# Kernel optimization log

Hardware: AMD Instinct MI355X
Metric: run time of the kernel (lower is better)

Reference implementation:

```python
import jax, jax.numpy as jnp
import numpy as np

N_NODES = 100000
N_FEATS = 256
OUT_DIM = 64
NNZ_X = 1280000
N_EDGES = 1600000
KEEP_PROB = 0.9  # 1 - dropout_rate (dropout_rate = 0.1)


def setup_inputs() -> dict:
    key = jax.random.key(0)
    ks = jax.random.split(key, 7)
    feat_values = jax.random.normal(ks[0], (NNZ_X,), dtype=jnp.float32)
    feat_rows = jax.random.randint(ks[1], (NNZ_X,), 0, N_NODES, dtype=jnp.int32)
    feat_cols = jax.random.randint(ks[2], (NNZ_X,), 0, N_FEATS, dtype=jnp.int32)
    # GlorotNormal kernel: std = sqrt(2 / (fan_in + fan_out))
    glorot_std = float(np.sqrt(2.0 / (N_FEATS + OUT_DIM)))
    kernel = jax.random.normal(ks[3], (N_FEATS, OUT_DIM), dtype=jnp.float32) * glorot_std
    adj_values = jax.random.uniform(ks[4], (N_EDGES,), dtype=jnp.float32)
    adj_rows = jax.random.randint(ks[5], (N_EDGES,), 0, N_NODES, dtype=jnp.int32)
    adj_cols = jax.random.randint(ks[6], (N_EDGES,), 0, N_NODES, dtype=jnp.int32)
    return {
        "feat_values": feat_values,
        "kernel": kernel,
        "adj_values": adj_values,
        "feat_rows": feat_rows,
        "feat_cols": feat_cols,
        "adj_rows": adj_rows,
        "adj_cols": adj_cols,
    }


def reference(feat_values, kernel, adj_values, feat_rows, feat_cols, adj_rows, adj_cols):
    # sparse dropout on feature values (training=True path), deterministic key.
    # tf: keep = floor(keep_prob + U[0,1)) cast to bool; retain then scale 1/keep_prob
    u = jax.random.uniform(jax.random.key(42), feat_values.shape, dtype=feat_values.dtype)
    keep = jnp.floor(KEEP_PROB + u).astype(bool)
    v = jnp.where(keep, feat_values, jnp.zeros_like(feat_values)) * (1.0 / KEEP_PROB)

    # SpMM 1: XW[n, o] = sum_{(n,f) in X} v * kernel[f, o]
    xw = jax.ops.segment_sum(v[:, None] * kernel[feat_cols], feat_rows,
                             num_segments=N_NODES)  # [N, OUT]

    # SpMM 2: out[i, o] = sum_{(i,j) in A} a_ij * xw[j, o]
    agg = jax.ops.segment_sum(adj_values[:, None] * xw[adj_cols], adj_rows,
                              num_segments=N_NODES)  # [N, OUT]

    return jax.nn.relu(agg)
```

## Files before the change

### kernel.cpp

```cpp
#include <hip/hip_runtime.h>

#define N_NODES 100000
#define N_FEATS 256
#define OUT_DIM 64
#define NNZ_X   1280000
#define N_EDGES 1600000
#define NB      391
#define CHUNK   4096
#define KPT     8
#define CAPX    4352
#define CAPA    5120

__device__ __forceinline__ unsigned rotl32(unsigned x, unsigned d) {
    return (x << d) | (x >> (32u - d));
}

__device__ __forceinline__ float jax_uniform_42(unsigned e) {
    unsigned x0 = 0u, x1 = e;
    const unsigned ks0 = 0u, ks1 = 42u, ks2 = 0u ^ 42u ^ 0x1BD11BDAu;
    x0 += ks0; x1 += ks1;
#define TF_R(r) { x0 += x1; x1 = rotl32(x1, r); x1 ^= x0; }
    TF_R(13) TF_R(15) TF_R(26) TF_R(6)
    x0 += ks1; x1 += ks2 + 1u;
    TF_R(17) TF_R(29) TF_R(16) TF_R(24)
    x0 += ks2; x1 += ks0 + 2u;
    TF_R(13) TF_R(15) TF_R(26) TF_R(6)
    x0 += ks0; x1 += ks1 + 3u;
    TF_R(17) TF_R(29) TF_R(16) TF_R(24)
    x0 += ks1; x1 += ks2 + 4u;
    TF_R(13) TF_R(15) TF_R(26) TF_R(6)
    x0 += ks2; x1 += ks0 + 5u;
#undef TF_R
    unsigned bits = x0 ^ x1;
    return __uint_as_float((bits >> 9) | 0x3f800000u) - 1.0f;
}

__device__ __forceinline__ bool keep_42(unsigned e) {
    float u = jax_uniform_42(e);
    return floorf(0.9f + u) != 0.0f;
}

__device__ __forceinline__ unsigned short f32_bf16(float f) {
    unsigned bits = __float_as_uint(f);
    return (unsigned short)((bits + 0x7fffu + ((bits >> 16) & 1u)) >> 16);
}

__device__ __forceinline__ float bf16_f32(unsigned short u) {
    return __uint_as_float((unsigned)u << 16);
}

__device__ __forceinline__ float bflo(unsigned u) { return __uint_as_float(u << 16); }
__device__ __forceinline__ float bfhi(unsigned u) { return __uint_as_float(u & 0xffff0000u); }

__global__ __launch_bounds__(512) void phase1(
        const float* __restrict__ fvals, const int* __restrict__ frows,
        const int* __restrict__ fcols,
        const float* __restrict__ avals, const int* __restrict__ arows,
        const int* __restrict__ acols,
        int* __restrict__ bcur_x, int* __restrict__ bcur_a,
        float2* __restrict__ gx, float2* __restrict__ ga) {
    const int isA = blockIdx.y;
    const float* vals = isA ? avals : fvals;
    const int* rows   = isA ? arows : frows;
    const int* cols   = isA ? acols : fcols;
    int* bcur         = isA ? bcur_a : bcur_x;
    float2* dst       = isA ? ga : gx;
    const unsigned cap = isA ? CAPA : CAPX;
    const unsigned n  = isA ? N_EDGES : NNZ_X;

    unsigned t = threadIdx.x;
    unsigned base = blockIdx.x * CHUNK;
    if (base >= n) return;

    __shared__ int cnt[512];
    __shared__ int start[512];
    __shared__ int cur[512];
    __shared__ int gbase[NB];
    __shared__ int wtot[8];
    __shared__ int s_nvalid;
    __shared__ unsigned long long payload[CHUNK];
    __shared__ unsigned short bkt[CHUNK];

    int   rcache[KPT];
    float vcache[KPT];
    int   ccache[KPT];

    cnt[t] = 0;
    __syncthreads();
    #pragma unroll
    for (int k = 0; k < KPT; k++) {
        unsigned i = base + k * 512u + t;
        int r = -1;
        if (i < n) {
            int rr = rows[i];
            float v = vals[i];
            int   c = cols[i];
            if (isA || keep_42(i)) {
                r = rr;
                vcache[k] = isA ? v : v * (float)(1.0 / 0.9);
                ccache[k] = c;
            }
        }
        rcache[k] = r;
        if (r >= 0) atomicAdd(&cnt[(unsigned)r >> 8], 1);
    }
    __syncthreads();
    unsigned lane = t & 63u, wid = t >> 6;
    int binv = cnt[t];
    int inc = binv;
    #pragma unroll
    for (int d = 1; d < 64; d <<= 1) {
        int v = __shfl_up(inc, d, 64);
        if (lane >= (unsigned)d) inc += v;
    }
    if (lane == 63u) wtot[wid] = inc;
    __syncthreads();
    int offw = 0;
    #pragma unroll
    for (int w = 0; w < 8; w++) if ((unsigned)w < wid) offw += wtot[w];
    int excl = offw + inc - binv;
    start[t] = excl;
    cur[t]   = excl;
    if (t == 511u) s_nvalid = excl + binv;
    if (t < NB) {
        int cb = cnt[t];
        if (cb > 0) gbase[t] = atomicAdd(&bcur[t], cb);
    }
    __syncthreads();
    int n_valid = s_nvalid;
    #pragma unroll
    for (int k = 0; k < KPT; k++) {
        int r = rcache[k];
        if (r >= 0) {
            unsigned b = (unsigned)r >> 8;
            int p = atomicAdd(&cur[b], 1);
            unsigned packed = ((unsigned)ccache[k] << 8) | ((unsigned)r & 255u);
            payload[p] = ((unsigned long long)__float_as_uint(vcache[k]) << 32) | packed;
            bkt[p] = (unsigned short)b;
        }
    }
    __syncthreads();
    #pragma unroll
    for (int k = 0; k < KPT; k++) {
        int sidx = k * 512 + (int)t;
        if (sidx < n_valid) {
            unsigned b = bkt[sidx];
            unsigned long long m = payload[sidx];
            float2 e;
            e.x = __uint_as_float((unsigned)(m >> 32));
            e.y = __int_as_float((int)(unsigned)m);
            dst[(size_t)b * cap + gbase[b] + (sidx - start[b])] = e;
        }
    }
}

__global__ __launch_bounds__(512) void sort_stage(
        const int* __restrict__ bcur_x, const float2* __restrict__ gx,
        const float* __restrict__ W, unsigned short* __restrict__ xw,
        const int* __restrict__ bcur_a, float2* __restrict__ ga,
        unsigned short* __restrict__ rs) {
    __shared__ float2 ent[CAPX];
    __shared__ int hist[256];
    __shared__ int starts[256];
    __shared__ int cursor[256];
    __shared__ int wtot[4];
    unsigned t = threadIdx.x;
    unsigned wid = t >> 6, lane = t & 63u;
    const int isA = (blockIdx.x >= NB);
    unsigned b = isA ? (blockIdx.x - NB) : blockIdx.x;

    if (!isA) {
        int cnt = bcur_x[b];
        const float2* src = gx + (size_t)b * CAPX;
        if (t < 256) hist[t] = 0;
        __syncthreads();
        for (int i = (int)t; i < cnt; i += 512)
            atomicAdd(&hist[((unsigned)__float_as_int(src[i].y)) & 255u], 1);
        __syncthreads();
        int inc = 0, binv = 0;
        if (wid < 4u) {
            unsigned bin = wid * 64u + lane;
            binv = hist[bin];
            inc = binv;
            #pragma unroll
            for (int d = 1; d < 64; d <<= 1) {
                int v = __shfl_up(inc, d, 64);
                if (lane >= (unsigned)d) inc += v;
            }
            if (lane == 63u) wtot[wid] = inc;
        }
        __syncthreads();
        if (wid < 4u) {
            int offw = 0;
            #pragma unroll
            for (int w = 0; w < 4; w++) if ((unsigned)w < wid) offw += wtot[w];
            unsigned bin = wid * 64u + lane;
            int excl = inc - binv + offw;
            starts[bin] = excl;
            cursor[bin] = excl;
        }
        __syncthreads();
        for (int i = (int)t; i < cnt; i += 512) {
            float2 e = src[i];
            int pos = atomicAdd(&cursor[((unsigned)__float_as_int(e.y)) & 255u], 1);
            ent[pos] = e;
        }
        __syncthreads();
        unsigned quarter = lane >> 4, sub = lane & 15u;
        const float4* W4 = (const float4*)W;
        ushort4* xw4 = (ushort4*)xw;
        for (unsigned r = wid; r < 256u; r += 8u) {
            int s0 = starts[r];
            int s1 = (r == 255u) ? cnt : starts[r + 1];
            float4 acc[4];
            #pragma unroll
            for (int j = 0; j < 4; j++) { acc[j].x = acc[j].y = acc[j].z = acc[j].w = 0.0f; }
            int p = s0;
            for (; p + 16 <= s1; p += 16) {
                float2 e[4];
                #pragma unroll
                for (int j = 0; j < 4; j++) e[j] = ent[p + 4 * quarter + j];
                float4 w[4];
                #pragma unroll
                for (int j = 0; j < 4; j++)
                    w[j] = W4[(((unsigned)__float_as_int(e[j].y)) >> 8) * 16u + sub];
                #pragma unroll
                for (int j = 0; j < 4; j++) {
                    acc[j].x = fmaf(e[j].x, w[j].x, acc[j].x);
                    acc[j].y = fmaf(e[j].x, w[j].y, acc[j].y);
                    acc[j].z = fmaf(e[j].x, w[j].z, acc[j].z);
                    acc[j].w = fmaf(e[j].x, w[j].w, acc[j].w);
                }
            }
            for (int q = p + (int)quarter; q < s1; q += 4) {
                float2 e = ent[q];
                float4 w = W4[(((unsigned)__float_as_int(e.y)) >> 8) * 16u + sub];
                acc[0].x = fmaf(e.x, w.x, acc[0].x);
                acc[0].y = fmaf(e.x, w.y, acc[0].y);
                acc[0].z = fmaf(e.x, w.z, acc[0].z);
                acc[0].w = fmaf(e.x, w.w, acc[0].w);
            }
            float ax = (acc[0].x + acc[1].x) + (acc[2].x + acc[3].x);
            float ay = (acc[0].y + acc[1].y) + (acc[2].y + acc[3].y);
            float az = (acc[0].z + acc[1].z) + (acc[2].z + acc[3].z);
            float aw = (acc[0].w + acc[1].w) + (acc[2].w + acc[3].w);
            ax += __shfl(ax, (int)(lane ^ 16u), 64);
            ay += __shfl(ay, (int)(lane ^ 16u), 64);
            az += __shfl(az, (int)(lane ^ 16u), 64);
            aw += __shfl(aw, (int)(lane ^ 16u), 64);
            ax += __shfl(ax, (int)(lane ^ 32u), 64);
            ay += __shfl(ay, (int)(lane ^ 32u), 64);
            az += __shfl(az, (int)(lane ^ 32u), 64);
            aw += __shfl(aw, (int)(lane ^ 32u), 64);
            unsigned grow = (b << 8) + r;
            if (quarter == 0 && grow < N_NODES) {
                ushort4 o;
                o.x = f32_bf16(ax); o.y = f32_bf16(ay);
                o.z = f32_bf16(az); o.w = f32_bf16(aw);
                xw4[(size_t)grow * 16u + sub] = o;
            }
        }
    } else {
        int cnt = bcur_a[b];
        float2* g = ga + (size_t)b * CAPA;
        if (t < 256) hist[t] = 0;
        __syncthreads();
        float2 ec[10];
        #pragma unroll
        for (int k = 0; k < 10; k++) {
            int i = k * 512 + (int)t;
            if (i < cnt) {
                float2 e = g[i];
                ec[k] = e;
                atomicAdd(&hist[((unsigned)__float_as_int(e.y)) & 255u], 1);
            }
        }
        __syncthreads();
        int inc = 0, binv = 0;
        if (wid < 4u) {
            unsigned bin = wid * 64u + lane;
            binv = hist[bin];
            inc = binv;
            #pragma unroll
            for (int d = 1; d < 64; d <<= 1) {
                int v = __shfl_up(inc, d, 64);
                if (lane >= (unsigned)d) inc += v;
            }
            if (lane == 63u) wtot[wid] = inc;
        }
        __syncthreads();
        if (wid < 4u) {
            int offw = 0;
            #pragma unroll
            for (int w = 0; w < 4; w++) if ((unsigned)w < wid) offw += wtot[w];
            unsigned bin = wid * 64u + lane;
            int excl = inc - binv + offw;
            cursor[bin] = excl;
            rs[(b << 8) + bin] = (unsigned short)excl;
        }
        __syncthreads();
        #pragma unroll
        for (int k = 0; k < 10; k++) {
            int i = k * 512 + (int)t;
            if (i < cnt) {
                unsigned packed = (unsigned)__float_as_int(ec[k].y);
                int pos = atomicAdd(&cursor[packed & 255u], 1);
                float2 o; o.x = ec[k].x; o.y = __int_as_float((int)(packed >> 8));
                g[pos] = o;
            }
        }
    }
}

__global__ void spmm2(const int* __restrict__ bcur_a,
                      const unsigned short* __restrict__ rs_a,
                      const float2* __restrict__ ga,
                      const unsigned short* __restrict__ xw,
                      float* __restrict__ out) {
    unsigned row  = blockIdx.x * 4u + (threadIdx.x >> 6);
    unsigned lane = threadIdx.x & 63u;
    if (row >= N_NODES) return;
    unsigned b = row >> 8, rl = row & 255u;
    int cnt = bcur_a[b];
    const float2* ent = ga + (size_t)b * CAPA;
    int s0 = rs_a[row];
    int s1 = (rl == 255u) ? cnt : (int)rs_a[row + 1];
    unsigned oct = lane >> 3;
    unsigned sub = lane & 7u;
    const uint4* xw8 = (const uint4*)xw;

    float acc[8];
    #pragma unroll
    for (int j = 0; j < 8; j++) acc[j] = 0.0f;

    int p = s0 + (int)oct;
    for (; p + 8 < s1; p += 16) {
        float2 e0 = ent[p];
        float2 e1 = ent[p + 8];
        uint4 u0 = xw8[((unsigned)__float_as_int(e0.y)) * 8u + sub];
        uint4 u1 = xw8[((unsigned)__float_as_int(e1.y)) * 8u + sub];
        float v0 = e0.x, v1 = e1.x;
        acc[0] = fmaf(v0, bflo(u0.x), acc[0]);
        acc[1] = fmaf(v0, bfhi(u0.x), acc[1]);
        acc[2] = fmaf(v0, bflo(u0.y), acc[2]);
        acc[3] = fmaf(v0, bfhi(u0.y), acc[3]);
        acc[4] = fmaf(v0, bflo(u0.z), acc[4]);
        acc[5] = fmaf(v0, bfhi(u0.z), acc[5]);
        acc[6] = fmaf(v0, bflo(u0.w), acc[6]);
        acc[7] = fmaf(v0, bfhi(u0.w), acc[7]);
        acc[0] = fmaf(v1, bflo(u1.x), acc[0]);
        acc[1] = fmaf(v1, bfhi(u1.x), acc[1]);
        acc[2] = fmaf(v1, bflo(u1.y), acc[2]);
        acc[3] = fmaf(v1, bfhi(u1.y), acc[3]);
        acc[4] = fmaf(v1, bflo(u1.z), acc[4]);
        acc[5] = fmaf(v1, bfhi(u1.z), acc[5]);
        acc[6] = fmaf(v1, bflo(u1.w), acc[6]);
        acc[7] = fmaf(v1, bfhi(u1.w), acc[7]);
    }
    if (p < s1) {
        float2 e = ent[p];
        uint4 u = xw8[((unsigned)__float_as_int(e.y)) * 8u + sub];
        float v = e.x;
        acc[0] = fmaf(v, bflo(u.x), acc[0]);
        acc[1] = fmaf(v, bfhi(u.x), acc[1]);
        acc[2] = fmaf(v, bflo(u.y), acc[2]);
        acc[3] = fmaf(v, bfhi(u.y), acc[3]);
        acc[4] = fmaf(v, bflo(u.z), acc[4]);
        acc[5] = fmaf(v, bfhi(u.z), acc[5]);
        acc[6] = fmaf(v, bflo(u.w), acc[6]);
        acc[7] = fmaf(v, bfhi(u.w), acc[7]);
    }
    #pragma unroll
    for (int j = 0; j < 8; j++) {
        acc[j] += __shfl_xor(acc[j], 8, 64);
        acc[j] += __shfl_xor(acc[j], 16, 64);
        acc[j] += __shfl_xor(acc[j], 32, 64);
    }
    if (oct == 0) {
        float4 o0, o1;
        o0.x = fmaxf(acc[0], 0.0f);
        o0.y = fmaxf(acc[1], 0.0f);
        o0.z = fmaxf(acc[2], 0.0f);
        o0.w = fmaxf(acc[3], 0.0f);
        o1.x = fmaxf(acc[4], 0.0f);
        o1.y = fmaxf(acc[5], 0.0f);
        o1.z = fmaxf(acc[6], 0.0f);
        o1.w = fmaxf(acc[7], 0.0f);
        float4* op = (float4*)(out + (size_t)row * 64u + sub * 8u);
        op[0] = o0;
        op[1] = o1;
    }
}

extern "C" void kernel_launch(void* const* d_in, const int* in_sizes, int n_in,
                              void* d_out, int out_size, void* d_ws, size_t ws_size,
                              hipStream_t stream) {
    const float* feat_values = (const float*)d_in[0];
    const float* W           = (const float*)d_in[1];
    const float* adj_values  = (const float*)d_in[2];
    const int*   feat_rows   = (const int*)d_in[3];
    const int*   feat_cols   = (const int*)d_in[4];
    const int*   adj_rows    = (const int*)d_in[5];
    const int*   adj_cols    = (const int*)d_in[6];
    float* out = (float*)d_out;

    char* ws = (char*)d_ws;
    int* bcur_x = (int*)(ws + 0);
    int* bcur_a = (int*)(ws + 2048);
    unsigned short* rs_a = (unsigned short*)(ws + 4096);
    float2* gx  = (float2*)(ws + 204800);
    float2* ga  = (float2*)(ws + 13817856);
    unsigned short* xw = (unsigned short*)(ws + 29833216);

    hipMemsetAsync(ws, 0, 4096, stream);

    dim3 gp1((N_EDGES + CHUNK - 1) / CHUNK, 2);
    phase1<<<gp1, 512, 0, stream>>>(feat_values, feat_rows, feat_cols,
                                    adj_values, adj_rows, adj_cols,
                                    bcur_x, bcur_a, gx, ga);
    sort_stage<<<2 * NB, 512, 0, stream>>>(bcur_x, gx, W, xw, bcur_a, ga, rs_a);
    spmm2<<<(N_NODES + 3) / 4, 256, 0, stream>>>(bcur_a, rs_a, ga, xw, out);
}
```

Measured before the change: 184.3 us.

## Fuse adjacency bucket sort into SpMM2 via shared memory, split sort stages

```diff
diff --git a/kernel.cpp b/kernel.cpp
--- a/kernel.cpp
+++ b/kernel.cpp
@@ -45,10 +45,6 @@
     return (unsigned short)((bits + 0x7fffu + ((bits >> 16) & 1u)) >> 16);
 }
 
-__device__ __forceinline__ float bf16_f32(unsigned short u) {
-    return __uint_as_float((unsigned)u << 16);
-}
-
 __device__ __forceinline__ float bflo(unsigned u) { return __uint_as_float(u << 16); }
 __device__ __forceinline__ float bfhi(unsigned u) { return __uint_as_float(u & 0xffff0000u); }
 
@@ -154,11 +150,9 @@
     }
 }
 
-__global__ __launch_bounds__(512) void sort_stage(
+__global__ __launch_bounds__(1024) void sort_x_spmm1(
         const int* __restrict__ bcur_x, const float2* __restrict__ gx,
-        const float* __restrict__ W, unsigned short* __restrict__ xw,
-        const int* __restrict__ bcur_a, float2* __restrict__ ga,
-        unsigned short* __restrict__ rs) {
+        const float* __restrict__ W, unsigned short* __restrict__ xw) {
     __shared__ float2 ent[CAPX];
     __shared__ int hist[256];
     __shared__ int starts[256];
@@ -166,229 +160,245 @@
     __shared__ int wtot[4];
     unsigned t = threadIdx.x;
     unsigned wid = t >> 6, lane = t & 63u;
-    const int isA = (blockIdx.x >= NB);
-    unsigned b = isA ? (blockIdx.x - NB) : blockIdx.x;
-
-    if (!isA) {
-        int cnt = bcur_x[b];
-        const float2* src = gx + (size_t)b * CAPX;
-        if (t < 256) hist[t] = 0;
-        __syncthreads();
-        for (int i = (int)t; i < cnt; i += 512)
-            atomicAdd(&hist[((unsigned)__float_as_int(src[i].y)) & 255u], 1);
-        __syncthreads();
-        int inc = 0, binv = 0;
-        if (wid < 4u) {
-            unsigned bin = wid * 64u + lane;
-            binv = hist[bin];
-            inc = binv;
-            #pragma unroll
-            for (int d = 1; d < 64; d <<= 1) {
-                int v = __shfl_up(inc, d, 64);
-                if (lane >= (unsigned)d) inc += v;
-            }
-            if (lane == 63u) wtot[wid] = inc;
-        }
-        __syncthreads();
-        if (wid < 4u) {
-            int offw = 0;
-            #pragma unroll
-            for (int w = 0; w < 4; w++) if ((unsigned)w < wid) offw += wtot[w];
-            unsigned bin = wid * 64u + lane;
-            int excl = inc - binv + offw;
-            starts[bin] = excl;
-            cursor[bin] = excl;
-        }
-        __syncthreads();
-        for (int i = (int)t; i < cnt; i += 512) {
+    unsigned b = blockIdx.x;
+    int cnt = bcur_x[b];
+    const float2* src = gx + (size_t)b * CAPX;
+
+    if (t < 256) hist[t] = 0;
+    __syncthreads();
+    float2 ec[4];
+    #pragma unroll
+    for (int k = 0; k < 4; k++) {
+        int i = k * 1024 + (int)t;
+        if (i < cnt) {
             float2 e = src[i];
+            ec[k] = e;
+            atomicAdd(&hist[((unsigned)__float_as_int(e.y)) & 255u], 1);
+        }
+    }
+    for (int i = 4096 + (int)t; i < cnt; i += 1024)
+        atomicAdd(&hist[((unsigned)__float_as_int(src[i].y)) & 255u], 1);
+    __syncthreads();
+    int inc = 0, binv = 0;
+    if (wid < 4u) {
+        unsigned bin = wid * 64u + lane;
+        binv = hist[bin];
+        inc = binv;
+        #pragma unroll
+        for (int d = 1; d < 64; d <<= 1) {
+            int v = __shfl_up(inc, d, 64);
+            if (lane >= (unsigned)d) inc += v;
+        }
+        if (lane == 63u) wtot[wid] = inc;
+    }
+    __syncthreads();
+    if (wid < 4u) {
+        int offw = 0;
+        #pragma unroll
+        for (int w = 0; w < 4; w++) if ((unsigned)w < wid) offw += wtot[w];
+        unsigned bin = wid * 64u + lane;
+        int excl = inc - binv + offw;
+        starts[bin] = excl;
+        cursor[bin] = excl;
+    }
+    __syncthreads();
+    #pragma unroll
+    for (int k = 0; k < 4; k++) {
+        int i = k * 1024 + (int)t;
+        if (i < cnt) {
+            float2 e = ec[k];
             int pos = atomicAdd(&cursor[((unsigned)__float_as_int(e.y)) & 255u], 1);
             ent[pos] = e;
         }
-        __syncthreads();
-        unsigned quarter = lane >> 4, sub = lane & 15u;
-        const float4* W4 = (const float4*)W;
-        ushort4* xw4 = (ushort4*)xw;
-        for (unsigned r = wid; r < 256u; r += 8u) {
-            int s0 = starts[r];
-            int s1 = (r == 255u) ? cnt : starts[r + 1];
-            float4 acc[4];
+    }
+    for (int i = 4096 + (int)t; i < cnt; i += 1024) {
+        float2 e = src[i];
+        int pos = atomicAdd(&cursor[((unsigned)__float_as_int(e.y)) & 255u], 1);
+        ent[pos] = e;
+    }
+    __syncthreads();
+    unsigned quarter = lane >> 4, sub = lane & 15u;
+    const float4* W4 = (const float4*)W;
+    ushort4* xw4 = (ushort4*)xw;
+    for (unsigned r = wid; r < 256u; r += 16u) {
+        int s0 = starts[r];
+        int s1 = (r == 255u) ? cnt : starts[r + 1];
+        float4 acc[4];
+        #pragma unroll
+        for (int j = 0; j < 4; j++) { acc[j].x = acc[j].y = acc[j].z = acc[j].w = 0.0f; }
+        int p = s0;
+        for (; p + 16 <= s1; p += 16) {
+            float2 e[4];
             #pragma unroll
-            for (int j = 0; j < 4; j++) { acc[j].x = acc[j].y = acc[j].z = acc[j].w = 0.0f; }
-            int p = s0;
-            for (; p + 16 <= s1; p += 16) {
-                float2 e[4];
-                #pragma unroll
-                for (int j = 0; j < 4; j++) e[j] = ent[p + 4 * quarter + j];
-                float4 w[4];
-                #pragma unroll
-                for (int j = 0; j < 4; j++)
-                    w[j] = W4[(((unsigned)__float_as_int(e[j].y)) >> 8) * 16u + sub];
-                #pragma unroll
-                for (int j = 0; j < 4; j++) {
-                    acc[j].x = fmaf(e[j].x, w[j].x, acc[j].x);
-                    acc[j].y = fmaf(e[j].x, w[j].y, acc[j].y);
-                    acc[j].z = fmaf(e[j].x, w[j].z, acc[j].z);
-                    acc[j].w = fmaf(e[j].x, w[j].w, acc[j].w);
-                }
+            for (int j = 0; j < 4; j++) e[j] = ent[p + 4 * quarter + j];
+            float4 w[4];
+            #pragma unroll
+            for (int j = 0; j < 4; j++)
+                w[j] = W4[(((unsigned)__float_as_int(e[j].y)) >> 8) * 16u + sub];
+            #pragma unroll
+            for (int j = 0; j < 4; j++) {
+                acc[j].x = fmaf(e[j].x, w[j].x, acc[j].x);
+                acc[j].y = fmaf(e[j].x, w[j].y, acc[j].y);
+                acc[j].z = fmaf(e[j].x, w[j].z, acc[j].z);
+                acc[j].w = fmaf(e[j].x, w[j].w, acc[j].w);
             }
-            for (int q = p + (int)quarter; q < s1; q += 4) {
-                float2 e = ent[q];
-                float4 w = W4[(((unsigned)__float_as_int(e.y)) >> 8) * 16u + sub];
-                acc[0].x = fmaf(e.x, w.x, acc[0].x);
-                acc[0].y = fmaf(e.x, w.y, acc[0].y);
-                acc[0].z = fmaf(e.x, w.z, acc[0].z);
-                acc[0].w = fmaf(e.x, w.w, acc[0].w);
-            }
-            float ax = (acc[0].x + acc[1].x) + (acc[2].x + acc[3].x);
-            float ay = (acc[0].y + acc[1].y) + (acc[2].y + acc[3].y);
-            float az = (acc[0].z + acc[1].z) + (acc[2].z + acc[3].z);
-            float aw = (acc[0].w + acc[1].w) + (acc[2].w + acc[3].w);
-            ax += __shfl(ax, (int)(lane ^ 16u), 64);
-            ay += __shfl(ay, (int)(lane ^ 16u), 64);
-            az += __shfl(az, (int)(lane ^ 16u), 64);
-            aw += __shfl(aw, (int)(lane ^ 16u), 64);
-            ax += __shfl(ax, (int)(lane ^ 32u), 64);
-            ay += __shfl(ay, (int)(lane ^ 32u), 64);
-            az += __shfl(az, (int)(lane ^ 32u), 64);
-            aw += __shfl(aw, (int)(lane ^ 32u), 64);
-            unsigned grow = (b << 8) + r;
-            if (quarter == 0 && grow < N_NODES) {
-                ushort4 o;
-                o.x = f32_bf16(ax); o.y = f32_bf16(ay);
-                o.z = f32_bf16(az); o.w = f32_bf16(aw);
-                xw4[(size_t)grow * 16u + sub] = o;
-            }
-        }
-    } else {
-        int cnt = bcur_a[b];
-        float2* g = ga + (size_t)b * CAPA;
-        if (t < 256) hist[t] = 0;
-        __syncthreads();
-        float2 ec[10];
-        #pragma unroll
-        for (int k = 0; k < 10; k++) {
-            int i = k * 512 + (int)t;
-            if (i < cnt) {
-                float2 e = g[i];
-                ec[k] = e;
-                atomicAdd(&hist[((unsigned)__float_as_int(e.y)) & 255u], 1);
-            }
-        }
-        __syncthreads();
-        int inc = 0, binv = 0;
-        if (wid < 4u) {
-            unsigned bin = wid * 64u + lane;
-            binv = hist[bin];
-            inc = binv;
-            #pragma unroll
-            for (int d = 1; d < 64; d <<= 1) {
-                int v = __shfl_up(inc, d, 64);
-                if (lane >= (unsigned)d) inc += v;
-            }
-            if (lane == 63u) wtot[wid] = inc;
-        }
-        __syncthreads();
-        if (wid < 4u) {
-            int offw = 0;
-            #pragma unroll
-            for (int w = 0; w < 4; w++) if ((unsigned)w < wid) offw += wtot[w];
-            unsigned bin = wid * 64u + lane;
-            int excl = inc - binv + offw;
-            cursor[bin] = excl;
-            rs[(b << 8) + bin] = (unsigned short)excl;
-        }
-        __syncthreads();
-        #pragma unroll
-        for (int k = 0; k < 10; k++) {
-            int i = k * 512 + (int)t;
-            if (i < cnt) {
-                unsigned packed = (unsigned)__float_as_int(ec[k].y);
-                int pos = atomicAdd(&cursor[packed & 255u], 1);
-                float2 o; o.x = ec[k].x; o.y = __int_as_float((int)(packed >> 8));
-                g[pos] = o;
-            }
-        }
-    }
-}
-
-__global__ void spmm2(const int* __restrict__ bcur_a,
-                      const unsigned short* __restrict__ rs_a,
-                      const float2* __restrict__ ga,
-                      const unsigned short* __restrict__ xw,
-                      float* __restrict__ out) {
-    unsigned row  = blockIdx.x * 4u + (threadIdx.x >> 6);
-    unsigned lane = threadIdx.x & 63u;
-    if (row >= N_NODES) return;
-    unsigned b = row >> 8, rl = row & 255u;
+        }
+        for (int q = p + (int)quarter; q < s1; q += 4) {
+            float2 e = ent[q];
+            float4 w = W4[(((unsigned)__float_as_int(e.y)) >> 8) * 16u + sub];
+            acc[0].x = fmaf(e.x, w.x, acc[0].x);
+            acc[0].y = fmaf(e.x, w.y, acc[0].y);
+            acc[0].z = fmaf(e.x, w.z, acc[0].z);
+            acc[0].w = fmaf(e.x, w.w, acc[0].w);
+        }
+        float ax = (acc[0].x + acc[1].x) + (acc[2].x + acc[3].x);
+        float ay = (acc[0].y + acc[1].y) + (acc[2].y + acc[3].y);
+        float az = (acc[0].z + acc[1].z) + (acc[2].z + acc[3].z);
+        float aw = (acc[0].w + acc[1].w) + (acc[2].w + acc[3].w);
+        ax += __shfl(ax, (int)(lane ^ 16u), 64);
+        ay += __shfl(ay, (int)(lane ^ 16u), 64);
+        az += __shfl(az, (int)(lane ^ 16u), 64);
+        aw += __shfl(aw, (int)(lane ^ 16u), 64);
+        ax += __shfl(ax, (int)(lane ^ 32u), 64);
+        ay += __shfl(ay, (int)(lane ^ 32u), 64);
+        az += __shfl(az, (int)(lane ^ 32u), 64);
+        aw += __shfl(aw, (int)(lane ^ 32u), 64);
+        unsigned grow = (b << 8) + r;
+        if (quarter == 0 && grow < N_NODES) {
+            ushort4 o;
+            o.x = f32_bf16(ax); o.y = f32_bf16(ay);
+            o.z = f32_bf16(az); o.w = f32_bf16(aw);
+            xw4[(size_t)grow * 16u + sub] = o;
+        }
+    }
+}
+
+__global__ __launch_bounds__(1024) void sort_a_spmm2(
+        const int* __restrict__ bcur_a, const float2* __restrict__ ga,
+        const unsigned short* __restrict__ xw, float* __restrict__ out) {
+    __shared__ float2 ent[CAPA];
+    __shared__ int hist[256];
+    __shared__ int starts[256];
+    __shared__ int cursor[256];
+    __shared__ int wtot[4];
+    unsigned t = threadIdx.x;
+    unsigned wid = t >> 6, lane = t & 63u;
+    unsigned b = blockIdx.x;
     int cnt = bcur_a[b];
-    const float2* ent = ga + (size_t)b * CAPA;
-    int s0 = rs_a[row];
-    int s1 = (rl == 255u) ? cnt : (int)rs_a[row + 1];
-    unsigned oct = lane >> 3;
-    unsigned sub = lane & 7u;
+    const float2* src = ga + (size_t)b * CAPA;
+
+    if (t < 256) hist[t] = 0;
+    __syncthreads();
+    float2 ec[5];
+    #pragma unroll
+    for (int k = 0; k < 5; k++) {
+        int i = k * 1024 + (int)t;
+        if (i < cnt) {
+            float2 e = src[i];
+            ec[k] = e;
+            atomicAdd(&hist[((unsigned)__float_as_int(e.y)) & 255u], 1);
+        }
+    }
+    __syncthreads();
+    int inc = 0, binv = 0;
+    if (wid < 4u) {
+        unsigned bin = wid * 64u + lane;
+        binv = hist[bin];
+        inc = binv;
+        #pragma unroll
+        for (int d = 1; d < 64; d <<= 1) {
+            int v = __shfl_up(inc, d, 64);
+            if (lane >= (unsigned)d) inc += v;
+        }
+        if (lane == 63u) wtot[wid] = inc;
+    }
+    __syncthreads();
+    if (wid < 4u) {
+        int offw = 0;
+        #pragma unroll
+        for (int w = 0; w < 4; w++) if ((unsigned)w < wid) offw += wtot[w];
+        unsigned bin = wid * 64u + lane;
+        int excl = inc - binv + offw;
+        starts[bin] = excl;
+        cursor[bin] = excl;
+    }
+    __syncthreads();
+    #pragma unroll
+    for (int k = 0; k < 5; k++) {
+        int i = k * 1024 + (int)t;
+        if (i < cnt) {
+            float2 e = ec[k];
+            int pos = atomicAdd(&cursor[((unsigned)__float_as_int(e.y)) & 255u], 1);
+            ent[pos] = e;
+        }
+    }
+    __syncthreads();
+    unsigned oct = lane >> 3, sub = lane & 7u;
     const uint4* xw8 = (const uint4*)xw;
-
-    float acc[8];
-    #pragma unroll
-    for (int j = 0; j < 8; j++) acc[j] = 0.0f;
-
-    int p = s0 + (int)oct;
-    for (; p + 8 < s1; p += 16) {
-        float2 e0 = ent[p];
-        float2 e1 = ent[p + 8];
-        uint4 u0 = xw8[((unsigned)__float_as_int(e0.y)) * 8u + sub];
-        uint4 u1 = xw8[((unsigned)__float_as_int(e1.y)) * 8u + sub];
-        float v0 = e0.x, v1 = e1.x;
-        acc[0] = fmaf(v0, bflo(u0.x), acc[0]);
-        acc[1] = fmaf(v0, bfhi(u0.x), acc[1]);
-        acc[2] = fmaf(v0, bflo(u0.y), acc[2]);
-        acc[3] = fmaf(v0, bfhi(u0.y), acc[3]);
-        acc[4] = fmaf(v0, bflo(u0.z), acc[4]);
-        acc[5] = fmaf(v0, bfhi(u0.z), acc[5]);
-        acc[6] = fmaf(v0, bflo(u0.w), acc[6]);
-        acc[7] = fmaf(v0, bfhi(u0.w), acc[7]);
-        acc[0] = fmaf(v1, bflo(u1.x), acc[0]);
-        acc[1] = fmaf(v1, bfhi(u1.x), acc[1]);
-        acc[2] = fmaf(v1, bflo(u1.y), acc[2]);
-        acc[3] = fmaf(v1, bfhi(u1.y), acc[3]);
-        acc[4] = fmaf(v1, bflo(u1.z), acc[4]);
-        acc[5] = fmaf(v1, bfhi(u1.z), acc[5]);
-        acc[6] = fmaf(v1, bflo(u1.w), acc[6]);
-        acc[7] = fmaf(v1, bfhi(u1.w), acc[7]);
-    }
-    if (p < s1) {
-        float2 e = ent[p];
-        uint4 u = xw8[((unsigned)__float_as_int(e.y)) * 8u + sub];
-        float v = e.x;
-        acc[0] = fmaf(v, bflo(u.x), acc[0]);
-        acc[1] = fmaf(v, bfhi(u.x), acc[1]);
-        acc[2] = fmaf(v, bflo(u.y), acc[2]);
-        acc[3] = fmaf(v, bfhi(u.y), acc[3]);
-        acc[4] = fmaf(v, bflo(u.z), acc[4]);
-        acc[5] = fmaf(v, bfhi(u.z), acc[5]);
-        acc[6] = fmaf(v, bflo(u.w), acc[6]);
-        acc[7] = fmaf(v, bfhi(u.w), acc[7]);
-    }
-    #pragma unroll
-    for (int j = 0; j < 8; j++) {
-        acc[j] += __shfl_xor(acc[j], 8, 64);
-        acc[j] += __shfl_xor(acc[j], 16, 64);
-        acc[j] += __shfl_xor(acc[j], 32, 64);
-    }
-    if (oct == 0) {
-        float4 o0, o1;
-        o0.x = fmaxf(acc[0], 0.0f);
-        o0.y = fmaxf(acc[1], 0.0f);
-        o0.z = fmaxf(acc[2], 0.0f);
-        o0.w = fmaxf(acc[3], 0.0f);
-        o1.x = fmaxf(acc[4], 0.0f);
-        o1.y = fmaxf(acc[5], 0.0f);
-        o1.z = fmaxf(acc[6], 0.0f);
-        o1.w = fmaxf(acc[7], 0.0f);
-        float4* op = (float4*)(out + (size_t)row * 64u + sub * 8u);
-        op[0] = o0;
-        op[1] = o1;
+    for (unsigned r = wid; r < 256u; r += 16u) {
+        int s0 = starts[r];
+        int s1 = (r == 255u) ? cnt : starts[r + 1];
+        float acc[8];
+        #pragma unroll
+        for (int j = 0; j < 8; j++) acc[j] = 0.0f;
+        int p = s0 + (int)oct;
+        for (; p + 8 < s1; p += 16) {
+            float2 e0 = ent[p];
+            float2 e1 = ent[p + 8];
+            uint4 u0 = xw8[(((unsigned)__float_as_int(e0.y)) >> 8) * 8u + sub];
+            uint4 u1 = xw8[(((unsigned)__float_as_int(e1.y)) >> 8) * 8u + sub];
+            float v0 = e0.x, v1 = e1.x;
+            acc[0] = fmaf(v0, bflo(u0.x), acc[0]);
+            acc[1] = fmaf(v0, bfhi(u0.x), acc[1]);
+            acc[2] = fmaf(v0, bflo(u0.y), acc[2]);
+            acc[3] = fmaf(v0, bfhi(u0.y), acc[3]);
+            acc[4] = fmaf(v0, bflo(u0.z), acc[4]);
+            acc[5] = fmaf(v0, bfhi(u0.z), acc[5]);
+            acc[6] = fmaf(v0, bflo(u0.w), acc[6]);
+            acc[7] = fmaf(v0, bfhi(u0.w), acc[7]);
+            acc[0] = fmaf(v1, bflo(u1.x), acc[0]);
+            acc[1] = fmaf(v1, bfhi(u1.x), acc[1]);
+            acc[2] = fmaf(v1, bflo(u1.y), acc[2]);
+            acc[3] = fmaf(v1, bfhi(u1.y), acc[3]);
+            acc[4] = fmaf(v1, bflo(u1.z), acc[4]);
+            acc[5] = fmaf(v1, bfhi(u1.z), acc[5]);
+            acc[6] = fmaf(v1, bflo(u1.w), acc[6]);
+            acc[7] = fmaf(v1, bfhi(u1.w), acc[7]);
+        }
+        if (p < s1) {
+            float2 e = ent[p];
+            uint4 u = xw8[(((unsigned)__float_as_int(e.y)) >> 8) * 8u + sub];
+            float v = e.x;
+            acc[0] = fmaf(v, bflo(u.x), acc[0]);
+            acc[1] = fmaf(v, bfhi(u.x), acc[1]);
+            acc[2] = fmaf(v, bflo(u.y), acc[2]);
+            acc[3] = fmaf(v, bfhi(u.y), acc[3]);
+            acc[4] = fmaf(v, bflo(u.z), acc[4]);
+            acc[5] = fmaf(v, bfhi(u.z), acc[5]);
+            acc[6] = fmaf(v, bflo(u.w), acc[6]);
+            acc[7] = fmaf(v, bfhi(u.w), acc[7]);
+        }
+        #pragma unroll
+        for (int j = 0; j < 8; j++) {
+            acc[j] += __shfl_xor(acc[j], 8, 64);
+            acc[j] += __shfl_xor(acc[j], 16, 64);
+            acc[j] += __shfl_xor(acc[j], 32, 64);
+        }
+        unsigned grow = (b << 8) + r;
+        if (oct == 0 && grow < N_NODES) {
+            float4 o0, o1;
+            o0.x = fmaxf(acc[0], 0.0f);
+            o0.y = fmaxf(acc[1], 0.0f);
+            o0.z = fmaxf(acc[2], 0.0f);
+            o0.w = fmaxf(acc[3], 0.0f);
+            o1.x = fmaxf(acc[4], 0.0f);
+            o1.y = fmaxf(acc[5], 0.0f);
+            o1.z = fmaxf(acc[6], 0.0f);
+            o1.w = fmaxf(acc[7], 0.0f);
+            float4* op = (float4*)(out + (size_t)grow * 64u + sub * 8u);
+            op[0] = o0;
+            op[1] = o1;
+        }
     }
 }
 
@@ -407,7 +417,6 @@
     char* ws = (char*)d_ws;
     int* bcur_x = (int*)(ws + 0);
     int* bcur_a = (int*)(ws + 2048);
-    unsigned short* rs_a = (unsigned short*)(ws + 4096);
     float2* gx  = (float2*)(ws + 204800);
     float2* ga  = (float2*)(ws + 13817856);
     unsigned short* xw = (unsigned short*)(ws + 29833216);
@@ -418,6 +427,6 @@
     phase1<<<gp1, 512, 0, stream>>>(feat_values, feat_rows, feat_cols,
                                     adj_values, adj_rows, adj_cols,
                                     bcur_x, bcur_a, gx, ga);
-    sort_stage<<<2 * NB, 512, 0, stream>>>(bcur_x, gx, W, xw, bcur_a, ga, rs_a);
-    spmm2<<<(N_NODES + 3) / 4, 256, 0, stream>>>(bcur_a, rs_a, ga, xw, out);
-}
+    sort_x_spmm1<<<NB, 1024, 0, stream>>>(bcur_x, gx, W, xw);
+    sort_a_spmm2<<<NB, 1024, 0, stream>>>(bcur_a, ga, xw, out);
+}
```

Measured after the change: 179.9 us. -2.4%, faster.
